# Kernel optimization log

Hardware: AMD Instinct MI355X
Metric: run time of the kernel (lower is better)

The kernel has to match this reference:

```python
import jax, jax.numpy as jnp
import numpy as np

GAMMA = 0.1
B, IN_F, FEAT, NCLASS = 4096, 1024, 512, 1000
D = 4 * FEAT  # concatenated feature width


def setup_inputs() -> dict:
    key = jax.random.key(0)
    ks = jax.random.split(key, 9)
    s_in = 1.0 / np.sqrt(IN_F)
    return {
        "x": jax.random.normal(ks[0], (B, IN_F), jnp.float32),
        "x_90": jax.random.normal(ks[1], (B, IN_F), jnp.float32),
        "x_180": jax.random.normal(ks[2], (B, IN_F), jnp.float32),
        "x_270": jax.random.normal(ks[3], (B, IN_F), jnp.float32),
        "W_f": jax.random.uniform(ks[4], (FEAT, IN_F), jnp.float32, -s_in, s_in),
        "b_f": jax.random.uniform(ks[5], (FEAT,), jnp.float32, -s_in, s_in),
        "W_r": jax.random.uniform(ks[6], (FEAT, IN_F), jnp.float32, -s_in, s_in),
        "b_r": jax.random.uniform(ks[7], (FEAT,), jnp.float32, -s_in, s_in),
        "centers": jax.random.normal(ks[8], (NCLASS, D), jnp.float32),
    }


def _forward_feature(x, x90, x180, x270, W_f, b_f, W_r, b_r):
    f = jax.nn.relu(x @ W_f.T + b_f)
    f90 = jax.nn.relu(x90 @ W_r.T + b_r)
    f180 = jax.nn.relu(x180 @ W_r.T + b_r)
    f270 = jax.nn.relu(x270 @ W_r.T + b_r)
    return jnp.concatenate((f, f90, f180, f270), axis=1)  # [B, 4*FEAT]


def _distance_centers(feat, centers):
    # ||f - c||_2 via GEMM trick: ||f||^2 + ||c||^2 - 2 f.c  (same math as
    # the expand/subtract/square/sum/sqrt in the original, w/o B*C*D tensor)
    f2 = jnp.sum(feat * feat, axis=1, keepdims=True)        # [B, 1]
    c2 = jnp.sum(centers * centers, axis=1)                 # [C]
    d2 = f2 + c2[None, :] - 2.0 * (feat @ centers.T)        # [B, C]
    return jnp.sqrt(jnp.maximum(d2, 0.0))


def reference(x, x_90, x_180, x_270, W_f, b_f, W_r, b_r, centers):
    feat = _forward_feature(x, x_90, x_180, x_270, W_f, b_f, W_r, b_r)
    return _distance_centers(feat, centers) * (-GAMMA)  # [B, NCLASS]
```

## Files before the change

kernel.cpp:

```cpp
#include <hip/hip_runtime.h>
#include <hip/hip_bf16.h>

typedef unsigned char u8;
typedef unsigned short u16;
typedef unsigned int u32;
typedef unsigned long long u64;
typedef __attribute__((ext_vector_type(4))) short short4v;
typedef __attribute__((ext_vector_type(4))) float f32x4;
typedef __attribute__((ext_vector_type(2))) unsigned int u32x2;

#define BSZ   4096
#define INF   1024
#define FEAT  512
#define NCLS  1000
#define NPAD  1024
#define DTOT  2048
#define WSCL  16.0f
#define WDSC  0.0625f

__device__ __forceinline__ u16 f2bf(float f) {
  unsigned int x = __float_as_uint(f);
  x += 0x7fffu + ((x >> 16) & 1u);
  return (u16)(x >> 16);
}
__device__ __forceinline__ float bf2f(u16 h) {
  return __uint_as_float((unsigned int)h << 16);
}
__device__ __forceinline__ u32 pk_fp8x4(float a, float b, float c, float d) {
  u32 r = 0;
  asm("v_cvt_pk_fp8_f32 %0, %1, %2" : "+v"(r) : "v"(a), "v"(b));
  asm("v_cvt_pk_fp8_f32 %0, %1, %2 op_sel:[0,0,1]" : "+v"(r) : "v"(c), "v"(d));
  return r;
}
__device__ __forceinline__ float dec_fp8(u8 b) {
  const u32 s = b >> 7, e = (b >> 3) & 15u, m = b & 7u;
  float v = e ? __uint_as_float(((e + 120u) << 23) | (m << 20))
              : (float)m * (1.0f / 512.0f);
  return s ? -v : v;
}
__device__ __forceinline__ void gload_lds16(const void* g, void* l) {
  __builtin_amdgcn_global_load_lds(
      (const __attribute__((address_space(1))) void*)g,
      (__attribute__((address_space(3))) void*)l, 16, 0, 0);
}

__global__ __launch_bounds__(256) void cvt_prep(const float* __restrict__ x0,
                                                const float* __restrict__ x1,
                                                const float* __restrict__ x2,
                                                const float* __restrict__ x3,
                                                const float* __restrict__ W_f,
                                                const float* __restrict__ W_r,
                                                const float* __restrict__ cen,
                                                u8* __restrict__ Xq,
                                                u8* __restrict__ Wq,
                                                u8* __restrict__ Cb,
                                                float* __restrict__ c2) {
  const int b = blockIdx.x;
  const int t = threadIdx.x;
  if (b < 8192) {
    const int q = b >> 11;
    const int i = (b & 2047) * 256 + t;
    const float* in = (q & 2) ? ((q & 1) ? x3 : x2) : ((q & 1) ? x1 : x0);
    const float4* p = (const float4*)in;
    float4 a = p[2 * i], bb = p[2 * i + 1];
    u32x2 o;
    o[0] = pk_fp8x4(a.x, a.y, a.z, a.w);
    o[1] = pk_fp8x4(bb.x, bb.y, bb.z, bb.w);
    *(u32x2*)&Xq[(size_t)q * BSZ * INF + (size_t)i * 8] = o;
    return;
  }
  if (b < 8704) {
    const int half = (b - 8192) >> 8;
    const int i = ((b - 8192) & 255) * 256 + t;
    const float* in = half ? W_r : W_f;
    const float4* p = (const float4*)in;
    float4 a = p[2 * i], bb = p[2 * i + 1];
    u32x2 o;
    o[0] = pk_fp8x4(a.x * WSCL, a.y * WSCL, a.z * WSCL, a.w * WSCL);
    o[1] = pk_fp8x4(bb.x * WSCL, bb.y * WSCL, bb.z * WSCL, bb.w * WSCL);
    *(u32x2*)&Wq[(size_t)half * FEAT * INF + (size_t)i * 8] = o;
    return;
  }
  const int row = b - 8704;
  float s = 0.f;
  if (row < NCLS) {
    const float4* p = (const float4*)(cen + (size_t)row * DTOT) + 2 * t;
    float4 a = p[0], bb = p[1];
    u32x2 o;
    o[0] = pk_fp8x4(a.x, a.y, a.z, a.w);
    o[1] = pk_fp8x4(bb.x, bb.y, bb.z, bb.w);
    *(u32x2*)&Cb[(size_t)row * DTOT + t * 8] = o;
#pragma unroll
    for (int q = 0; q < 4; ++q) { float f = dec_fp8((u8)(o[0] >> (8 * q))); s += f * f; }
#pragma unroll
    for (int q = 0; q < 4; ++q) { float f = dec_fp8((u8)(o[1] >> (8 * q))); s += f * f; }
  } else {
    u32x2 z = {0, 0};
    *(u32x2*)&Cb[(size_t)row * DTOT + t * 8] = z;
  }
#pragma unroll
  for (int o = 32; o > 0; o >>= 1) s += __shfl_xor(s, o);
  __shared__ float red[4];
  if ((t & 63) == 0) red[t >> 6] = s;
  __syncthreads();
  if (t == 0) c2[row] = red[0] + red[1] + red[2] + red[3];
}

__global__ __launch_bounds__(256) void feat_gemm(const u8* __restrict__ Xq,
                                                 const u8* __restrict__ Wq,
                                                 const float* __restrict__ bf_,
                                                 const float* __restrict__ br_,
                                                 u8* __restrict__ Fb) {
  __shared__ u8 As[2][128 * 128];
  __shared__ u8 Bs[2][128 * 128];
  const int t = threadIdx.x;
  const int lane = t & 63;
  const int wid = t >> 6;
  const int wr = (wid >> 1) * 64;
  const int wc = (wid & 1) * 64;
  const int lid = blockIdx.x;
  const int swg = (lid & 7) * 64 + (lid >> 3);
  const int bm0 = (swg >> 4) * 128;
  const int n  = swg & 15;
  const int gc0 = n * 128;
  const int g = n >> 2;
  const int bn0 = (n & 3) * 128;
  const u8* A = Xq + (size_t)g * BSZ * INF;
  const u8* Bt = Wq + (g ? (size_t)FEAT * INF : 0);
  const float* bias = g ? br_ : bf_;

  const int r32 = t >> 3;
  const int c8 = t & 7;
  const int l15 = lane & 15;
  const int l4 = lane >> 4;

  f32x4 acc[4][4] = {};

  auto stage = [&](int buf, int k0) {
#pragma unroll
    for (int it = 0; it < 4; ++it) {
      const int row = it * 32 + r32;
      const int sc = (c8 ^ ((row >> 1) & 7)) << 4;
      gload_lds16(&A[(size_t)(bm0 + row) * INF + k0 + sc],
                  &As[buf][row * 128 + c8 * 16]);
      gload_lds16(&Bt[(size_t)(bn0 + row) * INF + k0 + sc],
                  &Bs[buf][row * 128 + c8 * 16]);
    }
  };
  auto comp = [&](int buf) {
#pragma unroll
    for (int ks = 0; ks < 4; ++ks) {
      const int g16 = ks * 2 + (l4 >> 1);
      const int h8 = (l4 & 1) << 3;
      long av[4], bv[4];
#pragma unroll
      for (int i = 0; i < 4; ++i) {
        const int row = wr + i * 16 + l15;
        av[i] = *(const long*)&As[buf][row * 128 + ((g16 ^ ((row >> 1) & 7)) << 4) + h8];
      }
#pragma unroll
      for (int j = 0; j < 4; ++j) {
        const int row = wc + j * 16 + l15;
        bv[j] = *(const long*)&Bs[buf][row * 128 + ((g16 ^ ((row >> 1) & 7)) << 4) + h8];
      }
#pragma unroll
      for (int i = 0; i < 4; ++i)
#pragma unroll
        for (int j = 0; j < 4; ++j)
          acc[i][j] = __builtin_amdgcn_mfma_f32_16x16x32_fp8_fp8(av[i], bv[j],
                                                                 acc[i][j], 0, 0, 0);
    }
  };

  stage(0, 0);
  __syncthreads();
  for (int k0 = 0; k0 < INF; k0 += 256) {
    stage(1, k0 + 128);
    comp(0);
    __syncthreads();
    if (k0 + 256 < INF) stage(0, k0 + 256);
    comp(1);
    __syncthreads();
  }

#pragma unroll
  for (int j = 0; j < 4; ++j) {
    const int col = gc0 + wc + j * 16 + l15;
    const float bval = bias[bn0 + wc + j * 16 + l15];
#pragma unroll
    for (int i = 0; i < 4; ++i) {
      const int rowb = bm0 + wr + i * 16 + l4 * 4;
      float v0 = fmaxf(acc[i][j][0] * WDSC + bval, 0.f);
      float v1 = fmaxf(acc[i][j][1] * WDSC + bval, 0.f);
      float v2 = fmaxf(acc[i][j][2] * WDSC + bval, 0.f);
      float v3 = fmaxf(acc[i][j][3] * WDSC + bval, 0.f);
      u32 pk = pk_fp8x4(v0, v1, v2, v3);
#pragma unroll
      for (int r = 0; r < 4; ++r)
        Fb[(size_t)(rowb + r) * DTOT + col] = (u8)(pk >> (8 * r));
    }
  }
}

__global__ __launch_bounds__(256) void dist_gemm_sk(const u8* __restrict__ Fb,
                                                    const u8* __restrict__ Cb,
                                                    u16* __restrict__ P) {
  __shared__ u8 As[2][128 * 128];
  __shared__ u8 Bs[2][128 * 128];
  const int t = threadIdx.x;
  const int lane = t & 63;
  const int wid = t >> 6;
  const int wr = (wid >> 1) * 64;
  const int wc = (wid & 1) * 64;
  const int lid = blockIdx.x;
  const int swg = (lid & 7) * 64 + (lid >> 3);
  const int n = swg & 7;
  const int kidx = (swg >> 3) & 1;
  const int bm0 = (swg >> 4) * 128;
  const int bn0 = n * 128;
  const int kbase = kidx * 1024;

  const int r32 = t >> 3;
  const int c8 = t & 7;
  const int l15 = lane & 15;
  const int l4 = lane >> 4;

  f32x4 acc[4][4] = {};

  auto stage = [&](int buf, int k0) {
#pragma unroll
    for (int it = 0; it < 4; ++it) {
      const int row = it * 32 + r32;
      const int sc = (c8 ^ ((row >> 1) & 7)) << 4;
      gload_lds16(&Fb[(size_t)(bm0 + row) * DTOT + k0 + sc],
                  &As[buf][row * 128 + c8 * 16]);
      gload_lds16(&Cb[(size_t)(bn0 + row) * DTOT + k0 + sc],
                  &Bs[buf][row * 128 + c8 * 16]);
    }
  };
  auto comp = [&](int buf) {
#pragma unroll
    for (int ks = 0; ks < 4; ++ks) {
      const int g16 = ks * 2 + (l4 >> 1);
      const int h8 = (l4 & 1) << 3;
      long av[4], bv[4];
#pragma unroll
      for (int i = 0; i < 4; ++i) {
        const int row = wr + i * 16 + l15;
        av[i] = *(const long*)&As[buf][row * 128 + ((g16 ^ ((row >> 1) & 7)) << 4) + h8];
      }
#pragma unroll
      for (int j = 0; j < 4; ++j) {
        const int row = wc + j * 16 + l15;
        bv[j] = *(const long*)&Bs[buf][row * 128 + ((g16 ^ ((row >> 1) & 7)) << 4) + h8];
      }
#pragma unroll
      for (int i = 0; i < 4; ++i)
#pragma unroll
        for (int j = 0; j < 4; ++j)
          acc[i][j] = __builtin_amdgcn_mfma_f32_16x16x32_fp8_fp8(av[i], bv[j],
                                                                 acc[i][j], 0, 0, 0);
    }
  };

  stage(0, kbase);
  __syncthreads();
  for (int k0 = kbase; k0 < kbase + 1024; k0 += 256) {
    stage(1, k0 + 128);
    comp(0);
    __syncthreads();
    if (k0 + 256 < kbase + 1024) stage(0, k0 + 256);
    comp(1);
    __syncthreads();
  }

  u16* Pk = P + (size_t)kidx * BSZ * NPAD;
#pragma unroll
  for (int j = 0; j < 4; ++j) {
    const int col = bn0 + wc + j * 16 + l15;
#pragma unroll
    for (int i = 0; i < 4; ++i) {
#pragma unroll
      for (int r = 0; r < 4; ++r) {
        const int row = bm0 + wr + i * 16 + l4 * 4 + r;
        Pk[(size_t)row * NPAD + col] = f2bf(acc[i][j][r]);
      }
    }
  }
}

__global__ __launch_bounds__(256) void combine(const u8* __restrict__ Fb,
                                               const u16* __restrict__ P,
                                               const float* __restrict__ c2,
                                               float* __restrict__ out) {
  const int row = blockIdx.x;
  const int t = threadIdx.x;
  u64 v = *(const u64*)&Fb[(size_t)row * DTOT + t * 8];
  float s = 0.f;
#pragma unroll
  for (int q = 0; q < 8; ++q) { float f = dec_fp8((u8)(v >> (8 * q))); s += f * f; }
#pragma unroll
  for (int o = 32; o > 0; o >>= 1) s += __shfl_xor(s, o);
  __shared__ float red[4];
  if ((t & 63) == 0) red[t >> 6] = s;
  __syncthreads();
  const float fv = red[0] + red[1] + red[2] + red[3];

  const int c = t * 4;
  if (c >= NCLS) return;
  const short4v p0 = *(const short4v*)&P[(size_t)row * NPAD + c];
  const short4v p1 = *(const short4v*)&P[(size_t)(BSZ + row) * NPAD + c];
  const float4 cv = *(const float4*)&c2[c];
  float4 o;
  o.x = -0.1f * sqrtf(fmaxf(fv + cv.x - 2.f * (bf2f((u16)p0[0]) + bf2f((u16)p1[0])), 0.f));
  o.y = -0.1f * sqrtf(fmaxf(fv + cv.y - 2.f * (bf2f((u16)p0[1]) + bf2f((u16)p1[1])), 0.f));
  o.z = -0.1f * sqrtf(fmaxf(fv + cv.z - 2.f * (bf2f((u16)p0[2]) + bf2f((u16)p1[2])), 0.f));
  o.w = -0.1f * sqrtf(fmaxf(fv + cv.w - 2.f * (bf2f((u16)p0[3]) + bf2f((u16)p1[3])), 0.f));
  *(float4*)&out[(size_t)row * NCLS + c] = o;
}

extern "C" void kernel_launch(void* const* d_in, const int* in_sizes, int n_in,
                              void* d_out, int out_size, void* d_ws, size_t ws_size,
                              hipStream_t stream) {
  const float* x    = (const float*)d_in[0];
  const float* x90  = (const float*)d_in[1];
  const float* x180 = (const float*)d_in[2];
  const float* x270 = (const float*)d_in[3];
  const float* W_f  = (const float*)d_in[4];
  const float* b_f  = (const float*)d_in[5];
  const float* W_r  = (const float*)d_in[6];
  const float* b_r  = (const float*)d_in[7];
  const float* cen  = (const float*)d_in[8];
  float* out = (float*)d_out;

  u8*  Xq = (u8*)d_ws;
  u8*  Wq = Xq + 4ull * BSZ * INF;
  u8*  Cb = Wq + 2ull * FEAT * INF;
  u8*  Fb = Cb + (size_t)NPAD * DTOT;
  u16* P  = (u16*)(Fb + (size_t)BSZ * DTOT);
  float* c2 = (float*)(P + 2ull * BSZ * NPAD);

  cvt_prep<<<9728, 256, 0, stream>>>(x, x90, x180, x270, W_f, W_r, cen,
                                     Xq, Wq, Cb, c2);
  feat_gemm<<<512, 256, 0, stream>>>(Xq, Wq, b_f, b_r, Fb);
  dist_gemm_sk<<<512, 256, 0, stream>>>(Fb, Cb, P);
  combine<<<BSZ, 256, 0, stream>>>(Fb, P, c2, out);
}
```

Baseline: 63.39 us.

## Switch fp8 GEMMs to int8 MFMA with per-tensor scaling

Inputs, weights, centers and intermediate features are now quantized to int8 with fixed per-tensor scales instead of fp8. Both GEMMs now use the 16x16x64 int8 MFMA with int32 accumulators, which covers twice the K depth per instruction and uses 16-byte LDS fragment loads. Results are rescaled in the epilogues. The aim is higher matrix-core throughput, at the cost of more conversion work in the prep kernel and accuracy risk from clamping at the fixed scales.

```diff
diff --git a/kernel.cpp b/kernel.cpp
--- a/kernel.cpp
+++ b/kernel.cpp
@@ -6,6 +6,7 @@
 typedef unsigned int u32;
 typedef unsigned long long u64;
 typedef __attribute__((ext_vector_type(4))) short short4v;
+typedef __attribute__((ext_vector_type(4))) int int4v;
 typedef __attribute__((ext_vector_type(4))) float f32x4;
 typedef __attribute__((ext_vector_type(2))) unsigned int u32x2;
 
@@ -15,8 +16,12 @@
 #define NCLS  1000
 #define NPAD  1024
 #define DTOT  2048
-#define WSCL  16.0f
-#define WDSC  0.0625f
+#define SX    32.0f
+#define SW    4096.0f
+#define SF    32.0f
+#define SC    24.0f
+#define INV_SXSW 7.62939453125e-6f
+#define INV_SFSC (1.0f / 768.0f)
 
 __device__ __forceinline__ u16 f2bf(float f) {
   unsigned int x = __float_as_uint(f);
@@ -26,17 +31,14 @@
 __device__ __forceinline__ float bf2f(u16 h) {
   return __uint_as_float((unsigned int)h << 16);
 }
-__device__ __forceinline__ u32 pk_fp8x4(float a, float b, float c, float d) {
-  u32 r = 0;
-  asm("v_cvt_pk_fp8_f32 %0, %1, %2" : "+v"(r) : "v"(a), "v"(b));
-  asm("v_cvt_pk_fp8_f32 %0, %1, %2 op_sel:[0,0,1]" : "+v"(r) : "v"(c), "v"(d));
-  return r;
-}
-__device__ __forceinline__ float dec_fp8(u8 b) {
-  const u32 s = b >> 7, e = (b >> 3) & 15u, m = b & 7u;
-  float v = e ? __uint_as_float(((e + 120u) << 23) | (m << 20))
-              : (float)m * (1.0f / 512.0f);
-  return s ? -v : v;
+__device__ __forceinline__ u32 pk_i8x4(float a, float b, float c, float d,
+                                       float s) {
+  int ia = (int)rintf(fminf(fmaxf(a * s, -127.f), 127.f));
+  int ib = (int)rintf(fminf(fmaxf(b * s, -127.f), 127.f));
+  int ic = (int)rintf(fminf(fmaxf(c * s, -127.f), 127.f));
+  int id = (int)rintf(fminf(fmaxf(d * s, -127.f), 127.f));
+  return (u32)(ia & 255) | ((u32)(ib & 255) << 8) |
+         ((u32)(ic & 255) << 16) | ((u32)(id & 255) << 24);
 }
 __device__ __forceinline__ void gload_lds16(const void* g, void* l) {
   __builtin_amdgcn_global_load_lds(
@@ -64,8 +66,8 @@
     const float4* p = (const float4*)in;
     float4 a = p[2 * i], bb = p[2 * i + 1];
     u32x2 o;
-    o[0] = pk_fp8x4(a.x, a.y, a.z, a.w);
-    o[1] = pk_fp8x4(bb.x, bb.y, bb.z, bb.w);
+    o[0] = pk_i8x4(a.x, a.y, a.z, a.w, SX);
+    o[1] = pk_i8x4(bb.x, bb.y, bb.z, bb.w, SX);
     *(u32x2*)&Xq[(size_t)q * BSZ * INF + (size_t)i * 8] = o;
     return;
   }
@@ -76,8 +78,8 @@
     const float4* p = (const float4*)in;
     float4 a = p[2 * i], bb = p[2 * i + 1];
     u32x2 o;
-    o[0] = pk_fp8x4(a.x * WSCL, a.y * WSCL, a.z * WSCL, a.w * WSCL);
-    o[1] = pk_fp8x4(bb.x * WSCL, bb.y * WSCL, bb.z * WSCL, bb.w * WSCL);
+    o[0] = pk_i8x4(a.x, a.y, a.z, a.w, SW);
+    o[1] = pk_i8x4(bb.x, bb.y, bb.z, bb.w, SW);
     *(u32x2*)&Wq[(size_t)half * FEAT * INF + (size_t)i * 8] = o;
     return;
   }
@@ -87,13 +89,19 @@
     const float4* p = (const float4*)(cen + (size_t)row * DTOT) + 2 * t;
     float4 a = p[0], bb = p[1];
     u32x2 o;
-    o[0] = pk_fp8x4(a.x, a.y, a.z, a.w);
-    o[1] = pk_fp8x4(bb.x, bb.y, bb.z, bb.w);
+    o[0] = pk_i8x4(a.x, a.y, a.z, a.w, SC);
+    o[1] = pk_i8x4(bb.x, bb.y, bb.z, bb.w, SC);
     *(u32x2*)&Cb[(size_t)row * DTOT + t * 8] = o;
 #pragma unroll
-    for (int q = 0; q < 4; ++q) { float f = dec_fp8((u8)(o[0] >> (8 * q))); s += f * f; }
-#pragma unroll
-    for (int q = 0; q < 4; ++q) { float f = dec_fp8((u8)(o[1] >> (8 * q))); s += f * f; }
+    for (int q = 0; q < 4; ++q) {
+      float f = (float)(int)(signed char)(o[0] >> (8 * q)) * (1.f / SC);
+      s += f * f;
+    }
+#pragma unroll
+    for (int q = 0; q < 4; ++q) {
+      float f = (float)(int)(signed char)(o[1] >> (8 * q)) * (1.f / SC);
+      s += f * f;
+    }
   } else {
     u32x2 z = {0, 0};
     *(u32x2*)&Cb[(size_t)row * DTOT + t * 8] = z;
@@ -134,7 +142,7 @@
   const int l15 = lane & 15;
   const int l4 = lane >> 4;
 
-  f32x4 acc[4][4] = {};
+  int4v acc[4][4] = {};
 
   auto stage = [&](int buf, int k0) {
 #pragma unroll
@@ -149,26 +157,26 @@
   };
   auto comp = [&](int buf) {
 #pragma unroll
-    for (int ks = 0; ks < 4; ++ks) {
-      const int g16 = ks * 2 + (l4 >> 1);
-      const int h8 = (l4 & 1) << 3;
-      long av[4], bv[4];
+    for (int kk = 0; kk < 2; ++kk) {
+      int4v av[4], bv[4];
 #pragma unroll
       for (int i = 0; i < 4; ++i) {
         const int row = wr + i * 16 + l15;
-        av[i] = *(const long*)&As[buf][row * 128 + ((g16 ^ ((row >> 1) & 7)) << 4) + h8];
+        const int c = (4 * kk + l4) ^ ((row >> 1) & 7);
+        av[i] = *(const int4v*)&As[buf][row * 128 + c * 16];
       }
 #pragma unroll
       for (int j = 0; j < 4; ++j) {
         const int row = wc + j * 16 + l15;
-        bv[j] = *(const long*)&Bs[buf][row * 128 + ((g16 ^ ((row >> 1) & 7)) << 4) + h8];
+        const int c = (4 * kk + l4) ^ ((row >> 1) & 7);
+        bv[j] = *(const int4v*)&Bs[buf][row * 128 + c * 16];
       }
 #pragma unroll
       for (int i = 0; i < 4; ++i)
 #pragma unroll
         for (int j = 0; j < 4; ++j)
-          acc[i][j] = __builtin_amdgcn_mfma_f32_16x16x32_fp8_fp8(av[i], bv[j],
-                                                                 acc[i][j], 0, 0, 0);
+          acc[i][j] = __builtin_amdgcn_mfma_i32_16x16x64_i8(av[i], bv[j],
+                                                            acc[i][j], 0, 0, 0);
     }
   };
 
@@ -190,11 +198,11 @@
 #pragma unroll
     for (int i = 0; i < 4; ++i) {
       const int rowb = bm0 + wr + i * 16 + l4 * 4;
-      float v0 = fmaxf(acc[i][j][0] * WDSC + bval, 0.f);
-      float v1 = fmaxf(acc[i][j][1] * WDSC + bval, 0.f);
-      float v2 = fmaxf(acc[i][j][2] * WDSC + bval, 0.f);
-      float v3 = fmaxf(acc[i][j][3] * WDSC + bval, 0.f);
-      u32 pk = pk_fp8x4(v0, v1, v2, v3);
+      float v0 = fmaxf((float)acc[i][j][0] * INV_SXSW + bval, 0.f);
+      float v1 = fmaxf((float)acc[i][j][1] * INV_SXSW + bval, 0.f);
+      float v2 = fmaxf((float)acc[i][j][2] * INV_SXSW + bval, 0.f);
+      float v3 = fmaxf((float)acc[i][j][3] * INV_SXSW + bval, 0.f);
+      u32 pk = pk_i8x4(v0, v1, v2, v3, SF);
 #pragma unroll
       for (int r = 0; r < 4; ++r)
         Fb[(size_t)(rowb + r) * DTOT + col] = (u8)(pk >> (8 * r));
@@ -225,7 +233,7 @@
   const int l15 = lane & 15;
   const int l4 = lane >> 4;
 
-  f32x4 acc[4][4] = {};
+  int4v acc[4][4] = {};
 
   auto stage = [&](int buf, int k0) {
 #pragma unroll
@@ -240,26 +248,26 @@
   };
   auto comp = [&](int buf) {
 #pragma unroll
-    for (int ks = 0; ks < 4; ++ks) {
-      const int g16 = ks * 2 + (l4 >> 1);
-      const int h8 = (l4 & 1) << 3;
-      long av[4], bv[4];
+    for (int kk = 0; kk < 2; ++kk) {
+      int4v av[4], bv[4];
 #pragma unroll
       for (int i = 0; i < 4; ++i) {
         const int row = wr + i * 16 + l15;
-        av[i] = *(const long*)&As[buf][row * 128 + ((g16 ^ ((row >> 1) & 7)) << 4) + h8];
+        const int c = (4 * kk + l4) ^ ((row >> 1) & 7);
+        av[i] = *(const int4v*)&As[buf][row * 128 + c * 16];
       }
 #pragma unroll
       for (int j = 0; j < 4; ++j) {
         const int row = wc + j * 16 + l15;
-        bv[j] = *(const long*)&Bs[buf][row * 128 + ((g16 ^ ((row >> 1) & 7)) << 4) + h8];
+        const int c = (4 * kk + l4) ^ ((row >> 1) & 7);
+        bv[j] = *(const int4v*)&Bs[buf][row * 128 + c * 16];
       }
 #pragma unroll
       for (int i = 0; i < 4; ++i)
 #pragma unroll
         for (int j = 0; j < 4; ++j)
-          acc[i][j] = __builtin_amdgcn_mfma_f32_16x16x32_fp8_fp8(av[i], bv[j],
-                                                                 acc[i][j], 0, 0, 0);
+          acc[i][j] = __builtin_amdgcn_mfma_i32_16x16x64_i8(av[i], bv[j],
+                                                            acc[i][j], 0, 0, 0);
     }
   };
 
@@ -283,7 +291,7 @@
 #pragma unroll
       for (int r = 0; r < 4; ++r) {
         const int row = bm0 + wr + i * 16 + l4 * 4 + r;
-        Pk[(size_t)row * NPAD + col] = f2bf(acc[i][j][r]);
+        Pk[(size_t)row * NPAD + col] = f2bf((float)acc[i][j][r] * INV_SFSC);
       }
     }
   }
@@ -298,7 +306,10 @@
   u64 v = *(const u64*)&Fb[(size_t)row * DTOT + t * 8];
   float s = 0.f;
 #pragma unroll
-  for (int q = 0; q < 8; ++q) { float f = dec_fp8((u8)(v >> (8 * q))); s += f * f; }
+  for (int q = 0; q < 8; ++q) {
+    float f = (float)((u32)(v >> (8 * q)) & 0xffu) * (1.f / SF);
+    s += f * f;
+  }
 #pragma unroll
   for (int o = 32; o > 0; o >>= 1) s += __shfl_xor(s, o);
   __shared__ float red[4];
```

Measured after the change: 55.79 us. -12.0%, faster.
